# Performance work log

Measured on AMD Instinct MI355X. Metric: run time of the kernel, lower is better.

## Reference

```python
import jax, jax.numpy as jnp
import numpy as np

N_NODES = 50000
N_EDGES = 800000
IN_CH = 128
OUT_CH = 64
HEADS = 4
NEG_SLOPE = 0.2  # PyG GATConv default


def setup_inputs() -> dict:
    key = jax.random.key(0)
    k1, k2, k3, k4, k5 = jax.random.split(key, 5)
    x = jax.random.normal(k1, (N_NODES, IN_CH), dtype=jnp.float32)
    edge_index = jax.random.randint(k2, (2, N_EDGES), 0, N_NODES, dtype=jnp.int64)
    W = jax.random.normal(k3, (HEADS * OUT_CH, IN_CH), dtype=jnp.float32) * (1.0 / np.sqrt(IN_CH))
    att_src = jax.random.normal(k4, (HEADS, OUT_CH), dtype=jnp.float32) * (1.0 / np.sqrt(OUT_CH))
    att_dst = jax.random.normal(k5, (HEADS, OUT_CH), dtype=jnp.float32) * (1.0 / np.sqrt(OUT_CH))
    bias = jnp.zeros((OUT_CH,), dtype=jnp.float32)
    return {"x": x, "edge_index": edge_index, "W": W,
            "att_src": att_src, "att_dst": att_dst, "bias": bias}


def reference(x, edge_index, W, att_src, att_dst, bias):
    # GAT2NO_NORM.forward in eval mode: dropout == identity.
    N = x.shape[0]
    H, C = att_src.shape
    # PyG GATConv adds self-loops by default.
    loop = jnp.arange(N, dtype=edge_index.dtype)
    src = jnp.concatenate([edge_index[0], loop])  # message source j
    dst = jnp.concatenate([edge_index[1], loop])  # message target i
    # Linear projection, reshape to heads: [N, H, C]
    h = (x @ W.T).reshape(N, H, C)
    # Per-node attention halves: [N, H]
    a_src = jnp.einsum('nhc,hc->nh', h, att_src)
    a_dst = jnp.einsum('nhc,hc->nh', h, att_dst)
    # Per-edge raw score, LeakyReLU: [E, H]
    e = jax.nn.leaky_relu(a_src[src] + a_dst[dst], NEG_SLOPE)
    # Segment (edge-)softmax over incoming edges of each dst node.
    m = jax.lax.stop_gradient(jax.ops.segment_max(e, dst, num_segments=N))
    ex = jnp.exp(e - m[dst])
    denom = jax.ops.segment_sum(ex, dst, num_segments=N)
    alpha = ex / denom[dst]  # self-loops guarantee denom > 0
    # Weighted scatter-sum of messages: [N, H, C]
    msg = h[src] * alpha[:, :, None]
    out = jax.ops.segment_sum(msg, dst, num_segments=N)
    # concat=False -> mean over heads, then bias, then ReLU (module wrapper)
    out = out.mean(axis=1) + bias
    return jax.nn.relu(out)
```

## Files before the change

### kernel.cpp

```cpp
#include <hip/hip_runtime.h>
#include <hip/hip_fp16.h>
#include <math.h>

#define N_NODES 50000
#define N_EDGES 800000
#define IN_CH 128
#define PROJ_CH 256
#define OUT_CH 64
#define HEADS 4
#define NEG_SLOPE 0.2f
#define NREP 8
#define CAP8 20
#define CAPT (NREP * CAP8)
#define PROJ_BLOCKS 782
#define GRID_BLOCKS 3125

typedef _Float16 f16x8 __attribute__((ext_vector_type(8)));
typedef _Float16 f16x4 __attribute__((ext_vector_type(4)));
typedef __fp16   hf2   __attribute__((ext_vector_type(2)));
typedef float    f32x4 __attribute__((ext_vector_type(4)));

__device__ __forceinline__ float leaky(float v) {
    return v > 0.f ? v : NEG_SLOPE * v;
}

__device__ __forceinline__ hf2 u32_as_h2(unsigned int u) {
    union { unsigned int u; hf2 h; } c; c.u = u; return c.h;
}

__global__ __launch_bounds__(256) void prep_kernel(
    const float* __restrict__ W, _Float16* __restrict__ Wh, int* __restrict__ cnt8)
{
    const int t = blockIdx.x * 256 + threadIdx.x;
    if (t < PROJ_CH * IN_CH) Wh[t] = (_Float16)W[t];
    if (t < NREP * N_NODES) cnt8[t] = 0;
}

__global__ __launch_bounds__(256) void mega_kernel(
    const float* __restrict__ x, const _Float16* __restrict__ Wh,
    const float* __restrict__ att_src, const float* __restrict__ att_dst,
    const int* __restrict__ ei, int* __restrict__ cnt8, unsigned short* __restrict__ csr8,
    _Float16* __restrict__ h, float* __restrict__ a_src, float* __restrict__ a_dst)
{
    __shared__ _Float16 xs[64 * 136];
    const int tid = threadIdx.x;
    const int bid = blockIdx.x;
    const int rep = bid & (NREP - 1);

    const int e = bid * 256 + tid;
    const int esrc = ei[e];
    const int edst = ei[N_EDGES + e];

    if (bid >= PROJ_BLOCKS) {
        int pos = atomicAdd(&cnt8[rep * N_NODES + edst], 1);
        if (pos < CAP8) csr8[((size_t)rep * N_NODES + edst) * CAP8 + pos] = (unsigned short)esrc;
        return;
    }

    const int w    = tid >> 6;
    const int lane = tid & 63;
    const int q    = lane >> 4;
    const int l15  = lane & 15;
    const int nb   = bid * 64;

    f16x8 B[4][4];
#pragma unroll
    for (int k0i = 0; k0i < 4; ++k0i)
#pragma unroll
        for (int n0i = 0; n0i < 4; ++n0i) {
            const int oc = w * 64 + n0i * 16 + l15;
            B[k0i][n0i] = *(const f16x8*)(Wh + (size_t)oc * IN_CH + k0i * 32 + q * 8);
        }

#pragma unroll
    for (int r = 0; r < 8; ++r) {
        int v   = r * 256 + tid;
        int row = v >> 5;
        int c4  = v & 31;
        int grow = nb + row;
        if (grow > N_NODES - 1) grow = N_NODES - 1;
        float4 xv = *(const float4*)(x + (size_t)grow * IN_CH + c4 * 4);
        f16x4 hv;
        hv[0] = (_Float16)xv.x; hv[1] = (_Float16)xv.y;
        hv[2] = (_Float16)xv.z; hv[3] = (_Float16)xv.w;
        *(f16x4*)&xs[row * 136 + c4 * 4] = hv;
    }
    __syncthreads();

    const int pos = atomicAdd(&cnt8[rep * N_NODES + edst], 1);

    f32x4 acc[4][4];
#pragma unroll
    for (int m0i = 0; m0i < 4; ++m0i)
#pragma unroll
        for (int n0i = 0; n0i < 4; ++n0i)
            acc[m0i][n0i] = (f32x4){0.f, 0.f, 0.f, 0.f};

#pragma unroll
    for (int k0i = 0; k0i < 4; ++k0i) {
        f16x8 A[4];
#pragma unroll
        for (int m0i = 0; m0i < 4; ++m0i)
            A[m0i] = *(const f16x8*)&xs[(m0i * 16 + l15) * 136 + k0i * 32 + q * 8];
#pragma unroll
        for (int n0i = 0; n0i < 4; ++n0i)
#pragma unroll
            for (int m0i = 0; m0i < 4; ++m0i)
                acc[m0i][n0i] = __builtin_amdgcn_mfma_f32_16x16x32_f16(
                    A[m0i], B[k0i][n0i], acc[m0i][n0i], 0, 0, 0);
    }

    float att_s[4], att_d[4];
#pragma unroll
    for (int n0i = 0; n0i < 4; ++n0i) {
        att_s[n0i] = att_src[w * 64 + n0i * 16 + l15];
        att_d[n0i] = att_dst[w * 64 + n0i * 16 + l15];
    }

#pragma unroll
    for (int m0i = 0; m0i < 4; ++m0i) {
        float vs[4], vd[4];
#pragma unroll
        for (int r = 0; r < 4; ++r) {
            float s = 0.f, d = 0.f;
#pragma unroll
            for (int n0i = 0; n0i < 4; ++n0i) {
                s = fmaf(acc[m0i][n0i][r], att_s[n0i], s);
                d = fmaf(acc[m0i][n0i][r], att_d[n0i], d);
            }
            vs[r] = s; vd[r] = d;
        }
#pragma unroll
        for (int off = 1; off < 16; off <<= 1) {
#pragma unroll
            for (int r = 0; r < 4; ++r) {
                vs[r] += __shfl_xor(vs[r], off, 64);
                vd[r] += __shfl_xor(vd[r], off, 64);
            }
        }
#pragma unroll
        for (int r = 0; r < 4; ++r) {
            int node = nb + m0i * 16 + q * 4 + r;
            if (l15 == 0 && node < N_NODES) {
                a_src[node * HEADS + w] = vs[r];
                a_dst[node * HEADS + w] = vd[r];
            }
        }
#pragma unroll
        for (int r = 0; r < 4; ++r) {
            int node = nb + m0i * 16 + q * 4 + r;
            if (node < N_NODES) {
#pragma unroll
                for (int n0i = 0; n0i < 4; ++n0i)
                    h[(size_t)node * PROJ_CH + w * 64 + n0i * 16 + l15] =
                        (_Float16)acc[m0i][n0i][r];
            }
        }
    }

    if (pos < CAP8) csr8[((size_t)rep * N_NODES + edst) * CAP8 + pos] = (unsigned short)esrc;
}

__global__ __launch_bounds__(256) void aggregate_kernel(
    const _Float16* __restrict__ h, const float* __restrict__ a_src,
    const float* __restrict__ a_dst, const int* __restrict__ cnt8,
    const unsigned short* __restrict__ csr8, const float* __restrict__ bias,
    float* __restrict__ out)
{
    const int tid  = threadIdx.x;
    const int wave = tid >> 6;
    const int l    = tid & 63;
    const int i    = blockIdx.x * 4 + wave;

    __shared__ float lw_all[4][(CAPT + 1) * 4];
    __shared__ int   lj_all[4][CAPT + 4];
    float* lw = lw_all[wave];
    int*   lj = lj_all[wave];

    const int gr = l >> 3;
    const int gk = l & 7;
    int nr_g = 0, base_g = 0, m = 0;
#pragma unroll
    for (int r = 0; r < NREP; ++r) {
        int c = cnt8[r * N_NODES + i];
        c = min(c, CAP8);
        if (r == gr) { nr_g = c; base_g = m; }
        m += c;
    }
    if (l == 0) lj[0] = i;
    {
        const size_t cbase = ((size_t)gr * N_NODES + i) * CAP8;
#pragma unroll
        for (int kk = 0; kk < CAP8; kk += 8) {
            int k = gk + kk;
            if (k < nr_g) lj[1 + base_g + k] = (int)csr8[cbase + k];
        }
    }

    const int h4   = l & 3;
    const float adh = a_dst[i * 4 + h4];

    float lsum = 0.f;
    {
        float ws = __expf(leaky(a_src[i * 4 + h4] + adh));
        if (l < 4) { lw[l] = ws; lsum = ws; }
    }

    const int erel = l >> 2;
    for (int p0 = 0; p0 < m; p0 += 16) {
        int e = p0 + erel;
        bool valid = e < m;
        int j = valid ? lj[e + 1] : 0;
        float w = 0.f;
        if (valid) w = __expf(leaky(a_src[j * 4 + h4] + adh));
        lsum += w;
        lw[(e + 1) * 4 + h4] = w;
    }
#pragma unroll
    for (int off = 4; off < 64; off <<= 1) lsum += __shfl_xor(lsum, off, 64);

    __syncthreads();

    const int half_ = l >> 5;
    const int jj    = l & 31;
    const int hd    = jj >> 3;
    const int m_total = m + 1;
    const uint4* hv = (const uint4*)h;

    float acc[8];
#pragma unroll
    for (int k = 0; k < 8; ++k) acc[k] = 0.f;

    for (int qq = 0; qq < m_total; qq += 16) {
        const int eb = qq + 8 * half_;
        int ia[8]; float wa[8];
#pragma unroll
        for (int k = 0; k < 8; ++k) {
            int e2 = eb + k;
            bool v = e2 < m_total;
            ia[k] = v ? e2 : 0;
            wa[k] = v ? lw[ia[k] * 4 + hd] : 0.f;
        }
        uint4 d[8];
#pragma unroll
        for (int k = 0; k < 8; ++k)
            d[k] = hv[(size_t)lj[ia[k]] * 32 + jj];

        hf2 wp[4];
#pragma unroll
        for (int pr = 0; pr < 4; ++pr)
            wp[pr] = __builtin_amdgcn_cvt_pkrtz(wa[2 * pr], wa[2 * pr + 1]);

#pragma unroll
        for (int pr = 0; pr < 4; ++pr) {
            const unsigned int* Aa = (const unsigned int*)&d[2 * pr];
            const unsigned int* Ab = (const unsigned int*)&d[2 * pr + 1];
#pragma unroll
            for (int k = 0; k < 4; ++k) {
                unsigned int lo = __builtin_amdgcn_perm(Ab[k], Aa[k], 0x05040100u);
                unsigned int hi = __builtin_amdgcn_perm(Ab[k], Aa[k], 0x07060302u);
                acc[2 * k]     = __builtin_amdgcn_fdot2(u32_as_h2(lo), wp[pr], acc[2 * k], false);
                acc[2 * k + 1] = __builtin_amdgcn_fdot2(u32_as_h2(hi), wp[pr], acc[2 * k + 1], false);
            }
        }
    }

#pragma unroll
    for (int k = 0; k < 8; ++k) acc[k] += __shfl_xor(acc[k], 32, 64);

    float linv = 1.f / __shfl(lsum, hd, 64);
#pragma unroll
    for (int k = 0; k < 8; ++k) {
        float r = acc[k] * linv;
        r += __shfl_xor(r, 8, 64);
        r += __shfl_xor(r, 16, 64);
        acc[k] = r;
    }

    if (l < 8) {
        float* op = out + (size_t)i * OUT_CH + l * 8;
        float4 o0, o1;
        o0.x = fmaxf(0.25f * acc[0] + bias[l * 8 + 0], 0.f);
        o0.y = fmaxf(0.25f * acc[1] + bias[l * 8 + 1], 0.f);
        o0.z = fmaxf(0.25f * acc[2] + bias[l * 8 + 2], 0.f);
        o0.w = fmaxf(0.25f * acc[3] + bias[l * 8 + 3], 0.f);
        o1.x = fmaxf(0.25f * acc[4] + bias[l * 8 + 4], 0.f);
        o1.y = fmaxf(0.25f * acc[5] + bias[l * 8 + 5], 0.f);
        o1.z = fmaxf(0.25f * acc[6] + bias[l * 8 + 6], 0.f);
        o1.w = fmaxf(0.25f * acc[7] + bias[l * 8 + 7], 0.f);
        *(float4*)op = o0;
        *((float4*)op + 1) = o1;
    }
}

extern "C" void kernel_launch(void* const* d_in, const int* in_sizes, int n_in,
                              void* d_out, int out_size, void* d_ws, size_t ws_size,
                              hipStream_t stream)
{
    const float* x       = (const float*)d_in[0];
    const int*   ei      = (const int*)d_in[1];
    const float* W       = (const float*)d_in[2];
    const float* att_src = (const float*)d_in[3];
    const float* att_dst = (const float*)d_in[4];
    const float* bias    = (const float*)d_in[5];
    float* out = (float*)d_out;

    _Float16* h  = (_Float16*)d_ws;
    float* asrc  = (float*)(h + (size_t)N_NODES * PROJ_CH);
    float* adst  = asrc + (size_t)N_NODES * HEADS;
    int*   cnt8  = (int*)(adst + (size_t)N_NODES * HEADS);
    unsigned short* csr8 = (unsigned short*)(cnt8 + NREP * N_NODES);
    _Float16* Wh = (_Float16*)(csr8 + (size_t)NREP * N_NODES * CAP8);

    hipLaunchKernelGGL(prep_kernel, dim3((NREP * N_NODES + 255) / 256), dim3(256), 0, stream,
                       W, Wh, cnt8);
    hipLaunchKernelGGL(mega_kernel, dim3(GRID_BLOCKS), dim3(256), 0, stream,
                       x, Wh, att_src, att_dst, ei, cnt8, csr8, h, asrc, adst);
    hipLaunchKernelGGL(aggregate_kernel, dim3(N_NODES / 4), dim3(256), 0, stream,
                       h, asrc, adst, cnt8, csr8, bias, out);
}
```

Measured before the change: 202.8 us.

## Fold edge bucketing into projection blocks and pre-scale neighbor offsets in aggregation

The mega kernel now runs only the 782 projection blocks, and each thread handles four edges: it issues their atomic slot reservations before the GEMM and writes the CSR entries afterwards. This replaces the separate edge-only blocks, cutting the block count and overlapping atomic latency with the MFMA work. The aggregation kernel stores neighbor indices pre-shifted into byte offsets and uses a head-major weight layout with zero-padded slots. That removes bounds checks and index multiplies from the inner gather loop and allows vectorized weight loads. In exchange, the projection blocks carry more atomics and more register pressure, and fewer blocks do the edge work.

```diff
diff --git a/kernel.cpp b/kernel.cpp
--- a/kernel.cpp
+++ b/kernel.cpp
@@ -12,8 +12,9 @@
 #define NREP 8
 #define CAP8 20
 #define CAPT (NREP * CAP8)
-#define PROJ_BLOCKS 782
-#define GRID_BLOCKS 3125
+#define SLOTS 192
+#define MEGA_BLOCKS 782
+#define EPB 1024
 
 typedef _Float16 f16x8 __attribute__((ext_vector_type(8)));
 typedef _Float16 f16x4 __attribute__((ext_vector_type(4)));
@@ -47,14 +48,16 @@
     const int bid = blockIdx.x;
     const int rep = bid & (NREP - 1);
 
-    const int e = bid * 256 + tid;
-    const int esrc = ei[e];
-    const int edst = ei[N_EDGES + e];
-
-    if (bid >= PROJ_BLOCKS) {
-        int pos = atomicAdd(&cnt8[rep * N_NODES + edst], 1);
-        if (pos < CAP8) csr8[((size_t)rep * N_NODES + edst) * CAP8 + pos] = (unsigned short)esrc;
-        return;
+    const int e0 = bid * EPB + tid;
+    int es[4], ed[4], pos[4];
+#pragma unroll
+    for (int r = 0; r < 4; ++r) {
+        const int e = e0 + r * 256;
+        const bool v = e < N_EDGES;
+        es[r] = v ? ei[e] : 0;
+        ed[r] = v ? ei[N_EDGES + e] : 0;
+        pos[r] = CAP8;
+        if (v) pos[r] = atomicAdd(&cnt8[rep * N_NODES + ed[r]], 1);
     }
 
     const int w    = tid >> 6;
@@ -87,8 +90,6 @@
     }
     __syncthreads();
 
-    const int pos = atomicAdd(&cnt8[rep * N_NODES + edst], 1);
-
     f32x4 acc[4][4];
 #pragma unroll
     for (int m0i = 0; m0i < 4; ++m0i)
@@ -158,7 +159,10 @@
         }
     }
 
-    if (pos < CAP8) csr8[((size_t)rep * N_NODES + edst) * CAP8 + pos] = (unsigned short)esrc;
+#pragma unroll
+    for (int r = 0; r < 4; ++r)
+        if (pos[r] < CAP8)
+            csr8[((size_t)rep * N_NODES + ed[r]) * CAP8 + pos[r]] = (unsigned short)es[r];
 }
 
 __global__ __launch_bounds__(256) void aggregate_kernel(
@@ -172,8 +176,8 @@
     const int l    = tid & 63;
     const int i    = blockIdx.x * 4 + wave;
 
-    __shared__ float lw_all[4][(CAPT + 1) * 4];
-    __shared__ int   lj_all[4][CAPT + 4];
+    __shared__ float lw_all[4][HEADS * SLOTS];
+    __shared__ int   lj_all[4][SLOTS];
     float* lw = lw_all[wave];
     int*   lj = lj_all[wave];
 
@@ -187,34 +191,41 @@
         if (r == gr) { nr_g = c; base_g = m; }
         m += c;
     }
-    if (l == 0) lj[0] = i;
+    if (l == 0) lj[0] = i << 9;
     {
         const size_t cbase = ((size_t)gr * N_NODES + i) * CAP8;
 #pragma unroll
         for (int kk = 0; kk < CAP8; kk += 8) {
             int k = gk + kk;
-            if (k < nr_g) lj[1 + base_g + k] = (int)csr8[cbase + k];
+            if (k < nr_g) lj[1 + base_g + k] = ((int)csr8[cbase + k]) << 9;
         }
     }
 
     const int h4   = l & 3;
     const float adh = a_dst[i * 4 + h4];
+    const char* ab = (const char*)a_src;
 
     float lsum = 0.f;
     {
         float ws = __expf(leaky(a_src[i * 4 + h4] + adh));
-        if (l < 4) { lw[l] = ws; lsum = ws; }
-    }
-
+        if (l < 4) { lw[l * SLOTS] = ws; lsum = ws; }
+    }
+
+    const int T  = m + 1;
+    const int Tp = (T + 15) & ~15;
     const int erel = l >> 2;
-    for (int p0 = 0; p0 < m; p0 += 16) {
-        int e = p0 + erel;
-        bool valid = e < m;
-        int j = valid ? lj[e + 1] : 0;
+    for (int s0 = 0; s0 < Tp - 1; s0 += 16) {
+        const int e = s0 + erel;
+        const bool valid = e < m;
         float w = 0.f;
-        if (valid) w = __expf(leaky(a_src[j * 4 + h4] + adh));
+        if (valid) {
+            int sj = lj[e + 1];
+            w = __expf(leaky(*(const float*)(ab + (sj >> 5) + h4 * 4) + adh));
+        } else if (h4 == 0) {
+            lj[e + 1] = 0;
+        }
         lsum += w;
-        lw[(e + 1) * 4 + h4] = w;
+        lw[h4 * SLOTS + e + 1] = w;
     }
 #pragma unroll
     for (int off = 4; off < 64; off <<= 1) lsum += __shfl_xor(lsum, off, 64);
@@ -224,32 +235,30 @@
     const int half_ = l >> 5;
     const int jj    = l & 31;
     const int hd    = jj >> 3;
-    const int m_total = m + 1;
-    const uint4* hv = (const uint4*)h;
+    const unsigned jjb = (unsigned)jj * 16u;
+    const char* hb = (const char*)h;
+    const float* lwh = lw + hd * SLOTS;
 
     float acc[8];
 #pragma unroll
     for (int k = 0; k < 8; ++k) acc[k] = 0.f;
 
-    for (int qq = 0; qq < m_total; qq += 16) {
+    for (int qq = 0; qq < Tp; qq += 16) {
         const int eb = qq + 8 * half_;
-        int ia[8]; float wa[8];
-#pragma unroll
-        for (int k = 0; k < 8; ++k) {
-            int e2 = eb + k;
-            bool v = e2 < m_total;
-            ia[k] = v ? e2 : 0;
-            wa[k] = v ? lw[ia[k] * 4 + hd] : 0.f;
-        }
+        int o[8];
+#pragma unroll
+        for (int k = 0; k < 8; ++k) o[k] = lj[eb + k];
         uint4 d[8];
 #pragma unroll
         for (int k = 0; k < 8; ++k)
-            d[k] = hv[(size_t)lj[ia[k]] * 32 + jj];
+            d[k] = *(const uint4*)(hb + ((unsigned)o[k] + jjb));
 
         hf2 wp[4];
 #pragma unroll
-        for (int pr = 0; pr < 4; ++pr)
-            wp[pr] = __builtin_amdgcn_cvt_pkrtz(wa[2 * pr], wa[2 * pr + 1]);
+        for (int pr = 0; pr < 4; ++pr) {
+            float2 wf = *(const float2*)&lwh[eb + 2 * pr];
+            wp[pr] = __builtin_amdgcn_cvt_pkrtz(wf.x, wf.y);
+        }
 
 #pragma unroll
         for (int pr = 0; pr < 4; ++pr) {
@@ -314,7 +323,7 @@
 
     hipLaunchKernelGGL(prep_kernel, dim3((NREP * N_NODES + 255) / 256), dim3(256), 0, stream,
                        W, Wh, cnt8);
-    hipLaunchKernelGGL(mega_kernel, dim3(GRID_BLOCKS), dim3(256), 0, stream,
+    hipLaunchKernelGGL(mega_kernel, dim3(MEGA_BLOCKS), dim3(256), 0, stream,
                        x, Wh, att_src, att_dst, ei, cnt8, csr8, h, asrc, adst);
     hipLaunchKernelGGL(aggregate_kernel, dim3(N_NODES / 4), dim3(256), 0, stream,
                        h, asrc, adst, cnt8, csr8, bias, out);
```

Measured after the change: 201.0 us. Within noise of the previous version (-0.9%).
